# Kernel optimization log

Hardware: AMD Instinct MI355X
Metric: run time of the kernel (lower is better)

## Reference

```python
import jax, jax.numpy as jnp
import numpy as np

IN_FEATURES = 2048
OUT_FEATURES = 2048
BLOCK_SIZE = 16
F_BLOCKS = (OUT_FEATURES + BLOCK_SIZE - 1) // BLOCK_SIZE  # 128
G_BLOCKS = (IN_FEATURES + BLOCK_SIZE - 1) // BLOCK_SIZE   # 128
BATCH = 4096


def setup_inputs() -> dict:
    key = jax.random.key(0)
    k1, k2, k3 = jax.random.split(key, 3)
    x = jax.random.normal(k1, (BATCH, IN_FEATURES), dtype=jnp.float32)
    # Xavier-uniform-ish scale for index vectors viewed as (f*g, block_size)
    limit = np.sqrt(6.0 / (F_BLOCKS * G_BLOCKS + BLOCK_SIZE)).astype(np.float32)
    index_vectors = jax.random.uniform(
        k2, (F_BLOCKS, G_BLOCKS, BLOCK_SIZE), dtype=jnp.float32,
        minval=-limit, maxval=limit)
    b = jax.random.normal(k3, (OUT_FEATURES,), dtype=jnp.float32) * 0.02
    return {"x": x, "index_vectors": index_vectors, "b": b}


def reference(x, index_vectors, b):
    batch = x.shape[0]
    padded_in = G_BLOCKS * BLOCK_SIZE
    padded_out = F_BLOCKS * BLOCK_SIZE
    if x.shape[1] < padded_in:
        x = jnp.pad(x, ((0, 0), (0, padded_in - x.shape[1])))
    x_blocks = x.reshape(batch, G_BLOCKS, BLOCK_SIZE)            # (B, g, b)
    # Batched FFT over all blocks at once (replaces the f*g python loop)
    fft_p = jnp.fft.fft(index_vectors, axis=-1)                  # (f, g, b) complex
    fft_x = jnp.fft.fft(x_blocks, axis=-1)                       # (B, g, b) complex
    # sum_j IFFT(P_ij * X_j) == IFFT(sum_j P_ij * X_j) by linearity of IFFT
    out_fft = jnp.einsum('fgb,Bgb->Bfb', fft_p, fft_x)           # (B, f, b) complex
    out_blocks = jnp.fft.ifft(out_fft, axis=-1).real             # (B, f, b)
    out = out_blocks.reshape(batch, padded_out)
    if padded_out > OUT_FEATURES:
        out = out[:, :OUT_FEATURES]
    return out + b
```

## Files before the change

### kernel.cpp

```cpp
#include <hip/hip_runtime.h>
#include <hip/hip_bf16.h>


#define M_DIM 4096
#define N_DIM 2048
#define K_DIM 2048
#define BK 64
#define NT (K_DIM / BK)
#define BUFSZ 49152

typedef __attribute__((ext_vector_type(8))) short bf16x8;
typedef __attribute__((ext_vector_type(4))) float f32x4;

typedef const __attribute__((address_space(1))) void gvoid_t;
typedef __attribute__((address_space(3))) void lvoid_t;

#define FENCE asm volatile("" ::: "memory")
#define BAR()  do { FENCE; __builtin_amdgcn_s_barrier(); FENCE; } while (0)
#define GLD(src, dst) __builtin_amdgcn_global_load_lds((gvoid_t*)(src), (lvoid_t*)(dst), 16, 0, 0)

#define STAGE_A(dst, src) (GLD((src) + 0 * 64 * K_DIM, (dst) + 0),     \
                           GLD((src) + 1 * 64 * K_DIM, (dst) + 8192),  \
                           GLD((src) + 2 * 64 * K_DIM, (dst) + 16384), \
                           GLD((src) + 3 * 64 * K_DIM, (dst) + 24576))
#define STAGE_B(dst, src) (GLD((src) + 0 * 64 * K_DIM, (dst) + 0),     \
                           GLD((src) + 1 * 64 * K_DIM, (dst) + 8192))

__device__ __forceinline__ unsigned int f2bf(float f) {
  unsigned int u = __float_as_uint(f);
  return (u + 0x7fffu + ((u >> 16) & 1u)) >> 16;
}

__global__ __launch_bounds__(256) void prep_kernel(const float* __restrict__ x,
                                                   const float* __restrict__ iv,
                                                   unsigned short* __restrict__ xb,
                                                   unsigned short* __restrict__ W) {
  int b = blockIdx.x;
  if (b < (M_DIM * K_DIM / 8) / 256) {
    int idx = b * 256 + threadIdx.x;
    const float4* x4 = (const float4*)x;
    float4 a = x4[idx * 2 + 0];
    float4 c = x4[idx * 2 + 1];
    uint4 o;
    o.x = f2bf(a.x) | (f2bf(a.y) << 16);
    o.y = f2bf(a.z) | (f2bf(a.w) << 16);
    o.z = f2bf(c.x) | (f2bf(c.y) << 16);
    o.w = f2bf(c.z) | (f2bf(c.w) << 16);
    ((uint4*)xb)[idx] = o;
  } else {
    int idx = (b - (M_DIM * K_DIM / 8) / 256) * 256 + threadIdx.x;
    int o  = idx >> 8;
    int i0 = (idx & 255) * 8;
    int f = o >> 4, t = o & 15;
    int g = i0 >> 4, u0 = i0 & 15;
    const float* row = iv + (f * 128 + g) * 16;
    unsigned int p[4];
#pragma unroll
    for (int j = 0; j < 4; ++j) {
      unsigned int lo = f2bf(row[(t - (u0 + 2 * j + 0)) & 15]);
      unsigned int hi = f2bf(row[(t - (u0 + 2 * j + 1)) & 15]);
      p[j] = lo | (hi << 16);
    }
    ((uint4*)W)[idx] = make_uint4(p[0], p[1], p[2], p[3]);
  }
}

__global__ __launch_bounds__(512, 2) void gemm_bias_kernel(const unsigned short* __restrict__ A,
                                                           const unsigned short* __restrict__ B,
                                                           const float* __restrict__ bias,
                                                           float* __restrict__ C) {
  __shared__ char lds[3 * BUFSZ];

  const int tid = threadIdx.x;
  const int l   = tid & 63;
  const int w   = tid >> 6;
  const int wm  = w >> 1;
  const int wn  = w & 1;

  const int orig = blockIdx.x;
  const int swz  = (orig & 7) * 32 + (orig >> 3);
  const int bm   = swz >> 4;
  const int bn   = swz & 15;

  f32x4 acc[4][4] = {};

  const int srow  = w * 8 + (l >> 3);
  const int sslot = (l & 7) ^ ((l >> 3) & 7);
  const unsigned short* Asrc0 = A + (size_t)(bm * 256 + srow) * K_DIM + sslot * 8;
  const unsigned short* Bsrc0 = B + (size_t)(bn * 128 + srow) * K_DIM + sslot * 8;

  const int fr = l & 15;
  const int rxor = (l & 7) << 4;
  const int aRow0 = (wm * 64 + fr) * 128;
  const int bRow0 = (wn * 64 + fr) * 128;
  const int swzcol0 = (0 * 64 + (l >> 4) * 16) ^ rxor;
  const int swzcol1 = (1 * 64 + (l >> 4) * 16) ^ rxor;

  bf16x8 fa0[4], fb0[4], fa1[4], fb1[4];

#define LDA(SA, SB, BUF, SWZ)                                           \
  do {                                                                  \
    const char* Ab_ = lds + (BUF) * BUFSZ;                              \
    const char* Bb_ = Ab_ + 32768;                                      \
    _Pragma("unroll")                                                   \
    for (int m = 0; m < 4; ++m)                                         \
      SA[m] = *(const bf16x8*)(Ab_ + aRow0 + m * 2048 + (SWZ));         \
    _Pragma("unroll")                                                   \
    for (int n = 0; n < 4; ++n)                                         \
      SB[n] = *(const bf16x8*)(Bb_ + bRow0 + n * 2048 + (SWZ));         \
  } while (0)

#define MM(SA, SB, CNT)                                                 \
  do {                                                                  \
    asm volatile("s_waitcnt lgkmcnt(" #CNT ")" ::: "memory");           \
    __builtin_amdgcn_sched_barrier(0);                                  \
    __builtin_amdgcn_s_setprio(1);                                      \
    _Pragma("unroll")                                                   \
    for (int m = 0; m < 4; ++m)                                         \
      _Pragma("unroll")                                                 \
      for (int n = 0; n < 4; ++n)                                       \
        acc[m][n] = __builtin_amdgcn_mfma_f32_16x16x32_bf16(SA[m], SB[n], acc[m][n], 0, 0, 0); \
    __builtin_amdgcn_s_setprio(0);                                      \
    __builtin_amdgcn_sched_barrier(0);                                  \
  } while (0)

#define TILE_FULL(CUR, NXT, STG, T)                                     \
  do {                                                                  \
    LDA(fa1, fb1, CUR, swzcol1);                                        \
    STAGE_A(lds + (STG) * BUFSZ + w * 1024, Asrc0 + ((T) + 2) * BK);    \
    MM(fa0, fb0, 8);                                                    \
    asm volatile("s_waitcnt vmcnt(4)" ::: "memory");                    \
    BAR();                                                              \
    LDA(fa0, fb0, NXT, swzcol0);                                        \
    STAGE_B(lds + (STG) * BUFSZ + 32768 + w * 1024, Bsrc0 + ((T) + 2) * BK); \
    MM(fa1, fb1, 8);                                                    \
    BAR();                                                              \
  } while (0)

  STAGE_A(lds + 0 * BUFSZ + w * 1024, Asrc0 + 0 * BK);
  STAGE_B(lds + 0 * BUFSZ + 32768 + w * 1024, Bsrc0 + 0 * BK);
  STAGE_A(lds + 1 * BUFSZ + w * 1024, Asrc0 + 1 * BK);
  STAGE_B(lds + 1 * BUFSZ + 32768 + w * 1024, Bsrc0 + 1 * BK);
  asm volatile("s_waitcnt vmcnt(6)" ::: "memory");
  BAR();
  LDA(fa0, fb0, 0, swzcol0);

  for (int t = 0; t < NT - 2; t += 3) {
    TILE_FULL(0, 1, 2, t);
    TILE_FULL(1, 2, 0, t + 1);
    TILE_FULL(2, 0, 1, t + 2);
  }

  LDA(fa1, fb1, 0, swzcol1);
  MM(fa0, fb0, 8);
  asm volatile("s_waitcnt vmcnt(0)" ::: "memory");
  BAR();
  LDA(fa0, fb0, 1, swzcol0);
  MM(fa1, fb1, 8);
  LDA(fa1, fb1, 1, swzcol1);
  MM(fa0, fb0, 8);
  MM(fa1, fb1, 0);

  const int row0 = bm * 256 + wm * 64 + (l >> 4) * 4;
  const int col0 = bn * 128 + wn * 64 + (l & 15);
#pragma unroll
  for (int n = 0; n < 4; ++n) {
    float bv = bias[col0 + n * 16];
#pragma unroll
    for (int m = 0; m < 4; ++m) {
#pragma unroll
      for (int j = 0; j < 4; ++j) {
        C[(size_t)(row0 + m * 16 + j) * N_DIM + (col0 + n * 16)] = acc[m][n][j] + bv;
      }
    }
  }
#undef TILE_FULL
#undef MM
#undef LDA
}

__global__ __launch_bounds__(256) void fallback_kernel(const float* __restrict__ x,
                                                       const float* __restrict__ iv,
                                                       const float* __restrict__ b,
                                                       float* __restrict__ out) {
  int idx = blockIdx.x * 256 + threadIdx.x;
  int Bn = idx >> 11, o = idx & 2047;
  int f = o >> 4, t = o & 15;
  const float* xr = x + (size_t)Bn * 2048;
  float acc = 0.f;
  for (int g = 0; g < 128; ++g) {
    const float* pr = iv + (f * 128 + g) * 16;
    const float* xg = xr + g * 16;
#pragma unroll
    for (int s = 0; s < 16; ++s) acc += pr[s] * xg[(t - s) & 15];
  }
  out[idx] = acc + b[o];
}

extern "C" void kernel_launch(void* const* d_in, const int* in_sizes, int n_in,
                              void* d_out, int out_size, void* d_ws, size_t ws_size,
                              hipStream_t stream) {
  const float* x    = (const float*)d_in[0];
  const float* iv   = (const float*)d_in[1];
  const float* bias = (const float*)d_in[2];
  float* out = (float*)d_out;

  const size_t xb_bytes = (size_t)M_DIM * K_DIM * 2;
  const size_t w_bytes  = (size_t)N_DIM * K_DIM * 2;
  if (ws_size < xb_bytes + w_bytes) {
    fallback_kernel<<<(M_DIM * N_DIM) / 256, 256, 0, stream>>>(x, iv, bias, out);
    return;
  }

  unsigned short* xb = (unsigned short*)d_ws;
  unsigned short* W  = xb + (size_t)M_DIM * K_DIM;

  const int cvt_blocks = (M_DIM * K_DIM / 8) / 256;
  const int bw_blocks  = (N_DIM * K_DIM / 8) / 256;
  prep_kernel<<<cvt_blocks + bw_blocks, 256, 0, stream>>>(x, iv, xb, W);

  gemm_bias_kernel<<<(M_DIM / 256) * (N_DIM / 128), 512, 0, stream>>>(xb, W, bias, out);
}
```

Before: 55.10 us.

## Replace register double-buffered fragments with single-buffer load-then-MFMA phases

Drops the double-buffered register fragments (fa0/fb0, fa1/fb1), where the LDS reads for the next half-tile overlapped the current MFMA cluster. Each phase now loads its fragments, issues the global-to-LDS stage, waits on barriers, drains lgkmcnt to zero, then runs the MFMAs. This frees fragment registers and simplifies the schedule, but no longer hides LDS read latency behind compute inside a wave and adds barriers per phase.

```diff
diff --git a/kernel.cpp b/kernel.cpp
--- a/kernel.cpp
+++ b/kernel.cpp
@@ -96,45 +96,53 @@
   const int swzcol0 = (0 * 64 + (l >> 4) * 16) ^ rxor;
   const int swzcol1 = (1 * 64 + (l >> 4) * 16) ^ rxor;
 
-  bf16x8 fa0[4], fb0[4], fa1[4], fb1[4];
-
-#define LDA(SA, SB, BUF, SWZ)                                           \
+  bf16x8 fa[4], fb[4];
+
+#define LDA(BUF, SWZ)                                                   \
   do {                                                                  \
     const char* Ab_ = lds + (BUF) * BUFSZ;                              \
     const char* Bb_ = Ab_ + 32768;                                      \
     _Pragma("unroll")                                                   \
     for (int m = 0; m < 4; ++m)                                         \
-      SA[m] = *(const bf16x8*)(Ab_ + aRow0 + m * 2048 + (SWZ));         \
+      fa[m] = *(const bf16x8*)(Ab_ + aRow0 + m * 2048 + (SWZ));         \
     _Pragma("unroll")                                                   \
     for (int n = 0; n < 4; ++n)                                         \
-      SB[n] = *(const bf16x8*)(Bb_ + bRow0 + n * 2048 + (SWZ));         \
-  } while (0)
-
-#define MM(SA, SB, CNT)                                                 \
-  do {                                                                  \
-    asm volatile("s_waitcnt lgkmcnt(" #CNT ")" ::: "memory");           \
+      fb[n] = *(const bf16x8*)(Bb_ + bRow0 + n * 2048 + (SWZ));         \
+  } while (0)
+
+#define MFMA_CLUSTER()                                                  \
+  do {                                                                  \
+    asm volatile("s_waitcnt lgkmcnt(0)" ::: "memory");                  \
     __builtin_amdgcn_sched_barrier(0);                                  \
     __builtin_amdgcn_s_setprio(1);                                      \
     _Pragma("unroll")                                                   \
     for (int m = 0; m < 4; ++m)                                         \
       _Pragma("unroll")                                                 \
       for (int n = 0; n < 4; ++n)                                       \
-        acc[m][n] = __builtin_amdgcn_mfma_f32_16x16x32_bf16(SA[m], SB[n], acc[m][n], 0, 0, 0); \
+        acc[m][n] = __builtin_amdgcn_mfma_f32_16x16x32_bf16(fa[m], fb[n], acc[m][n], 0, 0, 0); \
     __builtin_amdgcn_s_setprio(0);                                      \
     __builtin_amdgcn_sched_barrier(0);                                  \
   } while (0)
 
-#define TILE_FULL(CUR, NXT, STG, T)                                     \
-  do {                                                                  \
-    LDA(fa1, fb1, CUR, swzcol1);                                        \
-    STAGE_A(lds + (STG) * BUFSZ + w * 1024, Asrc0 + ((T) + 2) * BK);    \
-    MM(fa0, fb0, 8);                                                    \
-    asm volatile("s_waitcnt vmcnt(4)" ::: "memory");                    \
+#define PHASE(BUF, SWZ, STAGE_STMT, VM_STMT)                            \
+  do {                                                                  \
+    LDA(BUF, SWZ);                                                      \
+    STAGE_STMT;                                                         \
+    VM_STMT;                                                            \
     BAR();                                                              \
-    LDA(fa0, fb0, NXT, swzcol0);                                        \
-    STAGE_B(lds + (STG) * BUFSZ + 32768 + w * 1024, Bsrc0 + ((T) + 2) * BK); \
-    MM(fa1, fb1, 8);                                                    \
+    MFMA_CLUSTER();                                                     \
     BAR();                                                              \
+  } while (0)
+
+#define VM6 asm volatile("s_waitcnt vmcnt(6)" ::: "memory")
+#define VM0 asm volatile("s_waitcnt vmcnt(0)" ::: "memory")
+#define NOSTAGE (void)0
+#define NOVM (void)0
+
+#define BODY(T, CUR, STG)                                               \
+  do {                                                                  \
+    PHASE(CUR, swzcol0, STAGE_A(lds + (STG) * BUFSZ + w * 1024, Asrc0 + ((T) + 2) * BK), NOVM); \
+    PHASE(CUR, swzcol1, STAGE_B(lds + (STG) * BUFSZ + 32768 + w * 1024, Bsrc0 + ((T) + 2) * BK), VM6); \
   } while (0)
 
   STAGE_A(lds + 0 * BUFSZ + w * 1024, Asrc0 + 0 * BK);
@@ -143,23 +151,19 @@
   STAGE_B(lds + 1 * BUFSZ + 32768 + w * 1024, Bsrc0 + 1 * BK);
   asm volatile("s_waitcnt vmcnt(6)" ::: "memory");
   BAR();
-  LDA(fa0, fb0, 0, swzcol0);
 
   for (int t = 0; t < NT - 2; t += 3) {
-    TILE_FULL(0, 1, 2, t);
-    TILE_FULL(1, 2, 0, t + 1);
-    TILE_FULL(2, 0, 1, t + 2);
-  }
-
-  LDA(fa1, fb1, 0, swzcol1);
-  MM(fa0, fb0, 8);
-  asm volatile("s_waitcnt vmcnt(0)" ::: "memory");
-  BAR();
-  LDA(fa0, fb0, 1, swzcol0);
-  MM(fa1, fb1, 8);
-  LDA(fa1, fb1, 1, swzcol1);
-  MM(fa0, fb0, 8);
-  MM(fa1, fb1, 0);
+    BODY(t + 0, 0, 2);
+    BODY(t + 1, 1, 0);
+    BODY(t + 2, 2, 1);
+  }
+
+  PHASE(0, swzcol0, NOSTAGE, NOVM);
+  PHASE(0, swzcol1, NOSTAGE, VM0);
+  LDA(1, swzcol0);
+  MFMA_CLUSTER();
+  LDA(1, swzcol1);
+  MFMA_CLUSTER();
 
   const int row0 = bm * 256 + wm * 64 + (l >> 4) * 4;
   const int col0 = bn * 128 + wn * 64 + (l & 15);
@@ -174,9 +178,14 @@
       }
     }
   }
-#undef TILE_FULL
-#undef MM
+#undef BODY
+#undef PHASE
+#undef MFMA_CLUSTER
 #undef LDA
+#undef VM6
+#undef VM0
+#undef NOSTAGE
+#undef NOVM
 }
 
 __global__ __launch_bounds__(256) void fallback_kernel(const float* __restrict__ x,
```

After: 56.81 us. 3.1% more time.
